# Performance work log

Measured on AMD Instinct MI355X. Metric: run time of the kernel, lower is better.

The kernel has to match this reference:

```python
import jax, jax.numpy as jnp
import numpy as np

INPUT_SIZE = 1024
HIDDEN_SIZE = 1024


def setup_inputs() -> dict:
    key = jax.random.key(0)
    k1, k2, k3 = jax.random.split(key, 3)
    x = jax.random.normal(k1, (512, 64, INPUT_SIZE), dtype=jnp.float32)
    weight_ih = jax.random.normal(k2, (INPUT_SIZE, HIDDEN_SIZE), dtype=jnp.float32)
    weight_hh = jax.random.normal(k3, (HIDDEN_SIZE, HIDDEN_SIZE), dtype=jnp.float32)
    return {"x": x, "weight_ih": weight_ih, "weight_hh": weight_hh}


def reference(x, weight_ih, weight_hh):
    # x: [T, B, input_size]; returns final hidden state [B, hidden_size]
    B = x.shape[1]
    h0 = jnp.zeros((B, weight_hh.shape[0]), dtype=x.dtype)

    def step(h, x_t):
        h = jnp.tanh(x_t @ weight_ih + h @ weight_hh)
        return h, None

    h_final, _ = jax.lax.scan(step, h0, x)
    return h_final
```

## Files before the change

### kernel.cpp

```cpp
#include <hip/hip_runtime.h>


#define TSTEPS 512
#define BATCH  64
#define HID    1024
#define NELEM  65536
#define LROW   1028

__device__ __forceinline__ float tanh_T2(float x) {
#pragma clang fp contract(off)
    const float C = 7.99881172180175781f;
    float ax = fabsf(x);
    float xc = fminf(fmaxf(x, -C), C);
    float x2 = xc * xc;
    float num = -2.76076847742355e-16f;
    num = __builtin_fmaf(x2, num, 2.00018790482477e-13f);
    num = __builtin_fmaf(x2, num, -8.60467152213735e-11f);
    num = __builtin_fmaf(x2, num, 5.12229709037114e-08f);
    num = __builtin_fmaf(x2, num, 1.48572235717979e-05f);
    num = __builtin_fmaf(x2, num, 6.37261928875436e-04f);
    num = __builtin_fmaf(x2, num, 4.89352455891786e-03f);
    num = xc * num;
    float den = 1.19825839466702e-06f;
    den = __builtin_fmaf(x2, den, 1.18534705686654e-04f);
    den = __builtin_fmaf(x2, den, 2.26843463243900e-03f);
    den = __builtin_fmaf(x2, den, 4.89352518554385e-03f);
    float r = num / den;
    return (ax < 0.0004f) ? x : r;
}

__global__ __launch_bounds__(256) void transpose_w(const float* __restrict__ W,
                                                   float* __restrict__ WT) {
    __shared__ float tile[64][65];
    const int c0 = blockIdx.x * 64;
    const int r0 = blockIdx.y * 64;
    const int tx = threadIdx.x & 63;
    const int ty = threadIdx.x >> 6;
    #pragma unroll
    for (int r = 0; r < 16; ++r) {
        const int rr = r * 4 + ty;
        tile[rr][tx] = W[(size_t)(r0 + rr) * HID + c0 + tx];
    }
    __syncthreads();
    #pragma unroll
    for (int r = 0; r < 16; ++r) {
        const int rr = r * 4 + ty;
        WT[(size_t)(c0 + rr) * HID + r0 + tx] = tile[tx][rr];
    }
}

__global__ __launch_bounds__(256, 2) void rnn_persist5(
    const float* __restrict__ x,
    const float* __restrict__ WTih,
    const float* __restrict__ WThh,
    float* __restrict__ hb0,
    float* __restrict__ hb1,
    unsigned int* __restrict__ cnt,
    float* __restrict__ out)
{
#pragma clang fp contract(off)
    __shared__ float lds_x[8 * LROW];
    __shared__ float lds_h[8 * LROW];
    __shared__ float pl[4][8][16];

    const int slice  = blockIdx.x & 7;
    const int wid    = blockIdx.x >> 3;
    const int bchunk = wid >> 3;
    const int jchunk = wid & 7;
    const int tid  = threadIdx.x;
    const int jl   = tid & 15;
    const int bp   = (tid >> 4) & 3;
    const int half = (tid >> 6) & 1;
    const int mat  = tid >> 7;
    const int jglob = slice * 128 + jchunk * 16 + jl;
    const int b0 = 2 * bp;

    const float* wrow = ((mat == 0) ? WTih : WThh)
                      + (size_t)jglob * HID + half * 512;
    float* hb[2] = { hb0, hb1 };
    unsigned int* mycnt = &cnt[bchunk * 32];

    for (int t = 0; t < TSTEPS; ++t) {
        float4 xv[8];
        {
            const float* xsrc = x + (size_t)t * NELEM
                              + (size_t)(bchunk * 8) * HID;
            #pragma unroll
            for (int u = 0; u < 8; ++u) {
                const int i = tid + u * 256;
                const int r = i >> 8, c4 = i & 255;
                xv[u] = ((const float4*)(xsrc + (size_t)r * HID))[c4];
            }
        }

        if (t > 0) {
            if (tid == 0) {
                const unsigned target = 64u * (unsigned)t;
                while (__hip_atomic_load(mycnt, __ATOMIC_RELAXED,
                                         __HIP_MEMORY_SCOPE_AGENT) < target)
                    __builtin_amdgcn_s_sleep(1);
            }
            __syncthreads();
        }

        #pragma unroll
        for (int u = 0; u < 8; ++u) {
            const int i = tid + u * 256;
            const int r = i >> 8, c4 = i & 255;
            *(float4*)&lds_x[r * LROW + c4 * 4] = xv[u];
        }
        if (t > 0) {
            const float* hsrc = hb[t & 1] + (size_t)(bchunk * 8) * HID;
            for (int blk = 0; blk < 4; ++blk) {
                float hv[8];
                #pragma unroll
                for (int u = 0; u < 8; ++u) {
                    const int i = tid + (blk * 8 + u) * 256;
                    const int r = i >> 10, k = i & 1023;
                    hv[u] = __hip_atomic_load(&hsrc[(size_t)r * HID + k],
                                              __ATOMIC_RELAXED,
                                              __HIP_MEMORY_SCOPE_AGENT);
                }
                #pragma unroll
                for (int u = 0; u < 8; ++u) {
                    const int i = tid + (blk * 8 + u) * 256;
                    const int r = i >> 10, k = i & 1023;
                    lds_h[r * LROW + k] = hv[u];
                }
            }
        }
        __syncthreads();

        float acc0 = 0.0f, acc1 = 0.0f;
        if (mat == 0 || t > 0) {
            const float* base = (mat == 0) ? lds_x : lds_h;
            const float* oa = base + b0 * LROW;
            const float* ob = base + (b0 + 1) * LROW;
            const float4* w4 = (const float4*)wrow;
            const int kbase = half * 512;
            #pragma unroll 4
            for (int kq = 0; kq < 128; ++kq) {
                const float4 w = w4[kq];
                const int k = kbase + kq * 4;
                acc0 = __builtin_fmaf(oa[k + 0], w.x, acc0);
                acc1 = __builtin_fmaf(ob[k + 0], w.x, acc1);
                acc0 = __builtin_fmaf(oa[k + 1], w.y, acc0);
                acc1 = __builtin_fmaf(ob[k + 1], w.y, acc1);
                acc0 = __builtin_fmaf(oa[k + 2], w.z, acc0);
                acc1 = __builtin_fmaf(ob[k + 2], w.z, acc1);
                acc0 = __builtin_fmaf(oa[k + 3], w.w, acc0);
                acc1 = __builtin_fmaf(ob[k + 3], w.w, acc1);
            }
        }
        pl[mat * 2 + half][b0][jl]     = acc0;
        pl[mat * 2 + half][b0 + 1][jl] = acc1;
        __syncthreads();

        if (tid < 128) {
            const int b = tid >> 4, j = tid & 15;
            const float dotX = pl[0][b][j] + pl[1][b][j];
            const float dotH = pl[2][b][j] + pl[3][b][j];
            const float hv = tanh_T2(dotX + dotH);
            const size_t o = (size_t)(bchunk * 8 + b) * HID
                           + (size_t)slice * 128 + (size_t)jchunk * 16 + j;
            if (t + 1 < TSTEPS)
                __hip_atomic_store(&hb[(t + 1) & 1][o], hv, __ATOMIC_RELAXED,
                                   __HIP_MEMORY_SCOPE_AGENT);
            else
                out[o] = hv;
        }
        __syncthreads();

        if (t + 1 < TSTEPS && tid == 0)
            __hip_atomic_fetch_add(mycnt, 1u, __ATOMIC_RELAXED,
                                   __HIP_MEMORY_SCOPE_AGENT);
    }
}

__global__ __launch_bounds__(256) void rnn_step_r8(
    const float* __restrict__ xt, const float* __restrict__ Wih,
    const float* __restrict__ Whh, const float* __restrict__ hin,
    float* __restrict__ hout)
{
#pragma clang fp contract(off)
    __shared__ float xs[4 * HID];
    __shared__ float hs[4 * HID];
    const int jb = blockIdx.x * 64;
    const int ib = blockIdx.y * 4;
    for (int idx = threadIdx.x; idx < 4 * HID; idx += 256) {
        xs[idx] = xt[ib * HID + idx];
        hs[idx] = hin ? hin[ib * HID + idx] : 0.0f;
    }
    __syncthreads();
    const int jl = threadIdx.x & 63;
    const int i  = threadIdx.x >> 6;
    const int j  = jb + jl;
    const float* xr = xs + i * HID;
    const float* hr = hs + i * HID;
    float cx0 = 0.f, cx1 = 0.f, ch0 = 0.f, ch1 = 0.f;
    #pragma unroll 8
    for (int k = 0; k < 512; ++k) {
        cx0 = __builtin_fmaf(xr[k], Wih[(size_t)k * HID + j], cx0);
        ch0 = __builtin_fmaf(hr[k], Whh[(size_t)k * HID + j], ch0);
    }
    #pragma unroll 8
    for (int k = 512; k < 1024; ++k) {
        cx1 = __builtin_fmaf(xr[k], Wih[(size_t)k * HID + j], cx1);
        ch1 = __builtin_fmaf(hr[k], Whh[(size_t)k * HID + j], ch1);
    }
    const float s = (cx0 + cx1) + (ch0 + ch1);
    hout[(size_t)(ib + i) * HID + j] = tanh_T2(s);
}

extern "C" void kernel_launch(void* const* d_in, const int* in_sizes, int n_in,
                              void* d_out, int out_size, void* d_ws, size_t ws_size,
                              hipStream_t stream) {
    const float* x   = (const float*)d_in[0];
    const float* Wih = (const float*)d_in[1];
    const float* Whh = (const float*)d_in[2];
    float* out = (float*)d_out;

    const size_t wT = (size_t)HID * HID;
    const size_t need = (2 * wT + 2 * (size_t)NELEM) * sizeof(float)
                      + 8 * 32 * sizeof(unsigned int);
    if (ws_size >= need) {
        float* WTih = (float*)d_ws;
        float* WThh = WTih + wT;
        float* hb0  = WThh + wT;
        float* hb1  = hb0 + NELEM;
        unsigned int* cnt = (unsigned int*)(hb1 + NELEM);

        transpose_w<<<dim3(16, 16), 256, 0, stream>>>(Wih, WTih);
        transpose_w<<<dim3(16, 16), 256, 0, stream>>>(Whh, WThh);
        hipMemsetAsync(cnt, 0, 8 * 32 * sizeof(unsigned int), stream);

        rnn_persist5<<<dim3(512), dim3(256), 0, stream>>>(
            x, WTih, WThh, hb0, hb1, cnt, out);
    } else {
        float* buf0 = (float*)d_ws;
        float* buf1 = buf0 + NELEM;
        const dim3 grid(HID / 64, BATCH / 4), block(256);
        for (int t = 0; t < TSTEPS; ++t) {
            const float* hin = (t == 0) ? nullptr
                              : ((t & 1) ? buf0 : buf1);
            float* hout = (t == TSTEPS - 1) ? out
                         : ((t & 1) ? buf1 : buf0);
            rnn_step_r8<<<grid, block, 0, stream>>>(
                x + (size_t)t * NELEM, Wih, Whh, hin, hout);
        }
    }
}
```

Before: 16.27 ms.

## Hoist input projection into a batched GEMM before the persistent recurrent kernel

Computes x_t @ W_ih for all timesteps up front in a separate parallel GEMM kernel, writing a large dotX buffer to workspace. The persistent recurrent kernel then only does the h @ W_hh matvec per step, reading precomputed dotX, with a new 256-block by 512-thread layout. This takes the input projection off the serial critical path, at the cost of 128MB of extra workspace traffic. The old per-step fallback is removed, and the previous persistent kernel now serves as the fallback when workspace is too small.

```diff
diff --git a/kernel.cpp b/kernel.cpp
--- a/kernel.cpp
+++ b/kernel.cpp
@@ -49,13 +49,166 @@
     }
 }
 
-__global__ __launch_bounds__(256, 2) void rnn_persist5(
+__global__ __launch_bounds__(256) void gemm_x(
     const float* __restrict__ x,
-    const float* __restrict__ WTih,
+    const float* __restrict__ Wih,
+    float* __restrict__ dotX)
+{
+#pragma clang fp contract(off)
+    __shared__ float xs[16 * LROW];
+
+    const int t  = blockIdx.z;
+    const int bc = blockIdx.y;
+    const int jb = blockIdx.x * 64;
+    const int tid = threadIdx.x;
+
+    {
+        const float* xsrc = x + (size_t)t * NELEM + (size_t)(bc * 16) * HID;
+        #pragma unroll
+        for (int s = 0; s < 16; ++s) {
+            const int f = tid + s * 256;
+            const int r = f >> 8, c4 = f & 255;
+            const float4 v = ((const float4*)(xsrc + (size_t)r * HID))[c4];
+            *(float4*)&xs[r * LROW + c4 * 4] = v;
+        }
+    }
+    __syncthreads();
+
+    const int jq = tid & 15;
+    const int i  = tid >> 4;
+    const int j0 = jb + jq * 4;
+    const float* xr = xs + i * LROW;
+
+    float a0[4] = {0.f, 0.f, 0.f, 0.f};
+    float a1[4] = {0.f, 0.f, 0.f, 0.f};
+    #pragma unroll 8
+    for (int k = 0; k < 512; ++k) {
+        const float4 w = *(const float4*)(Wih + (size_t)k * HID + j0);
+        const float xv = xr[k];
+        a0[0] = __builtin_fmaf(xv, w.x, a0[0]);
+        a0[1] = __builtin_fmaf(xv, w.y, a0[1]);
+        a0[2] = __builtin_fmaf(xv, w.z, a0[2]);
+        a0[3] = __builtin_fmaf(xv, w.w, a0[3]);
+    }
+    #pragma unroll 8
+    for (int k = 512; k < 1024; ++k) {
+        const float4 w = *(const float4*)(Wih + (size_t)k * HID + j0);
+        const float xv = xr[k];
+        a1[0] = __builtin_fmaf(xv, w.x, a1[0]);
+        a1[1] = __builtin_fmaf(xv, w.y, a1[1]);
+        a1[2] = __builtin_fmaf(xv, w.z, a1[2]);
+        a1[3] = __builtin_fmaf(xv, w.w, a1[3]);
+    }
+    float4 r;
+    r.x = a0[0] + a1[0];
+    r.y = a0[1] + a1[1];
+    r.z = a0[2] + a1[2];
+    r.w = a0[3] + a1[3];
+    *(float4*)(dotX + (size_t)t * NELEM + (size_t)(bc * 16 + i) * HID + j0) = r;
+}
+
+__global__ __launch_bounds__(512, 1) void rnn_persist7(
+    const float* __restrict__ dotX,
     const float* __restrict__ WThh,
     float* __restrict__ hb0,
     float* __restrict__ hb1,
     unsigned int* __restrict__ cnt,
+    float* __restrict__ out)
+{
+#pragma clang fp contract(off)
+    __shared__ float lds_h[8 * LROW];
+    __shared__ float pl[2][8][32];
+
+    const int xcd    = blockIdx.x & 7;
+    const int jsub   = (blockIdx.x >> 3) & 3;
+    const int bchunk = blockIdx.x >> 5;
+    const int tid  = threadIdx.x;
+    const int jl   = tid & 31;
+    const int b    = (tid >> 5) & 7;
+    const int half = tid >> 8;
+    const int jbase = xcd * 128 + jsub * 32;
+    const int j     = jbase + jl;
+
+    const float* wrow = WThh + (size_t)j * HID + half * 512;
+    float* hb[2] = { hb0, hb1 };
+    unsigned int* mycnt = &cnt[bchunk * 32];
+
+    for (int t = 0; t < TSTEPS; ++t) {
+        float dxv = 0.0f;
+        if (tid < 256) {
+            const int cb = tid >> 5, cj = tid & 31;
+            dxv = dotX[(size_t)t * NELEM + (size_t)(bchunk * 8 + cb) * HID
+                       + jbase + cj];
+        }
+
+        if (t > 0) {
+            if (tid == 0) {
+                const unsigned target = 32u * (unsigned)t;
+                while (__hip_atomic_load(mycnt, __ATOMIC_RELAXED,
+                                         __HIP_MEMORY_SCOPE_AGENT) < target)
+                    __builtin_amdgcn_s_sleep(1);
+            }
+            __syncthreads();
+
+            const float* hsrc = hb[t & 1] + (size_t)(bchunk * 8) * HID;
+            float hv[16];
+            #pragma unroll
+            for (int u = 0; u < 16; ++u) {
+                const int i = tid + u * 512;
+                const int r = i >> 10, k = i & 1023;
+                hv[u] = __hip_atomic_load(&hsrc[(size_t)r * HID + k],
+                                          __ATOMIC_RELAXED,
+                                          __HIP_MEMORY_SCOPE_AGENT);
+            }
+            #pragma unroll
+            for (int u = 0; u < 16; ++u) {
+                const int i = tid + u * 512;
+                const int r = i >> 10, k = i & 1023;
+                lds_h[r * LROW + k] = hv[u];
+            }
+        }
+        __syncthreads();
+
+        float acc = 0.0f;
+        if (t > 0) {
+            const float* hrow = lds_h + b * LROW + half * 512;
+            const float4* w4 = (const float4*)wrow;
+            #pragma unroll 4
+            for (int kq = 0; kq < 128; ++kq) {
+                const float4 w = w4[kq];
+                const int k = kq * 4;
+                acc = __builtin_fmaf(hrow[k + 0], w.x, acc);
+                acc = __builtin_fmaf(hrow[k + 1], w.y, acc);
+                acc = __builtin_fmaf(hrow[k + 2], w.z, acc);
+                acc = __builtin_fmaf(hrow[k + 3], w.w, acc);
+            }
+        }
+        pl[half][b][jl] = acc;
+        __syncthreads();
+
+        if (tid < 256) {
+            const int cb = tid >> 5, cj = tid & 31;
+            const float dotH = pl[0][cb][cj] + pl[1][cb][cj];
+            const float hv = tanh_T2(dxv + dotH);
+            const size_t o = (size_t)(bchunk * 8 + cb) * HID + jbase + cj;
+            if (t + 1 < TSTEPS)
+                __hip_atomic_store(&hb[(t + 1) & 1][o], hv, __ATOMIC_RELAXED,
+                                   __HIP_MEMORY_SCOPE_AGENT);
+            else
+                out[o] = hv;
+        }
+        __syncthreads();
+
+        if (t + 1 < TSTEPS && tid == 0)
+            __hip_atomic_fetch_add(mycnt, 1u, __ATOMIC_RELAXED,
+                                   __HIP_MEMORY_SCOPE_AGENT);
+    }
+}
+
+__global__ __launch_bounds__(256, 2) void rnn_persist5(
+    const float* __restrict__ x, const float* __restrict__ WTih,
+    const float* __restrict__ WThh, float* __restrict__ hb0,
+    float* __restrict__ hb1, unsigned int* __restrict__ cnt,
     float* __restrict__ out)
 {
 #pragma clang fp contract(off)
@@ -92,7 +245,6 @@
                 xv[u] = ((const float4*)(xsrc + (size_t)r * HID))[c4];
             }
         }
-
         if (t > 0) {
             if (tid == 0) {
                 const unsigned target = 64u * (unsigned)t;
@@ -102,7 +254,6 @@
             }
             __syncthreads();
         }
-
         #pragma unroll
         for (int u = 0; u < 8; ++u) {
             const int i = tid + u * 256;
@@ -177,41 +328,6 @@
     }
 }
 
-__global__ __launch_bounds__(256) void rnn_step_r8(
-    const float* __restrict__ xt, const float* __restrict__ Wih,
-    const float* __restrict__ Whh, const float* __restrict__ hin,
-    float* __restrict__ hout)
-{
-#pragma clang fp contract(off)
-    __shared__ float xs[4 * HID];
-    __shared__ float hs[4 * HID];
-    const int jb = blockIdx.x * 64;
-    const int ib = blockIdx.y * 4;
-    for (int idx = threadIdx.x; idx < 4 * HID; idx += 256) {
-        xs[idx] = xt[ib * HID + idx];
-        hs[idx] = hin ? hin[ib * HID + idx] : 0.0f;
-    }
-    __syncthreads();
-    const int jl = threadIdx.x & 63;
-    const int i  = threadIdx.x >> 6;
-    const int j  = jb + jl;
-    const float* xr = xs + i * HID;
-    const float* hr = hs + i * HID;
-    float cx0 = 0.f, cx1 = 0.f, ch0 = 0.f, ch1 = 0.f;
-    #pragma unroll 8
-    for (int k = 0; k < 512; ++k) {
-        cx0 = __builtin_fmaf(xr[k], Wih[(size_t)k * HID + j], cx0);
-        ch0 = __builtin_fmaf(hr[k], Whh[(size_t)k * HID + j], ch0);
-    }
-    #pragma unroll 8
-    for (int k = 512; k < 1024; ++k) {
-        cx1 = __builtin_fmaf(xr[k], Wih[(size_t)k * HID + j], cx1);
-        ch1 = __builtin_fmaf(hr[k], Whh[(size_t)k * HID + j], ch1);
-    }
-    const float s = (cx0 + cx1) + (ch0 + ch1);
-    hout[(size_t)(ib + i) * HID + j] = tanh_T2(s);
-}
-
 extern "C" void kernel_launch(void* const* d_in, const int* in_sizes, int n_in,
                               void* d_out, int out_size, void* d_ws, size_t ws_size,
                               hipStream_t stream) {
@@ -220,33 +336,36 @@
     const float* Whh = (const float*)d_in[2];
     float* out = (float*)d_out;
 
-    const size_t wT = (size_t)HID * HID;
-    const size_t need = (2 * wT + 2 * (size_t)NELEM) * sizeof(float)
-                      + 8 * 32 * sizeof(unsigned int);
-    if (ws_size >= need) {
+    const size_t dotX_f = (size_t)TSTEPS * NELEM;
+    const size_t wT_f   = (size_t)HID * HID;
+    const size_t need_new = (dotX_f + wT_f + 2 * (size_t)NELEM) * sizeof(float)
+                          + 8 * 32 * sizeof(unsigned int);
+    const size_t need_old = (2 * wT_f + 2 * (size_t)NELEM) * sizeof(float)
+                          + 8 * 32 * sizeof(unsigned int);
+
+    if (ws_size >= need_new) {
+        float* dotX = (float*)d_ws;
+        float* WThh = dotX + dotX_f;
+        float* hb0  = WThh + wT_f;
+        float* hb1  = hb0 + NELEM;
+        unsigned int* cnt = (unsigned int*)(hb1 + NELEM);
+
+        transpose_w<<<dim3(16, 16), 256, 0, stream>>>(Whh, WThh);
+        gemm_x<<<dim3(16, 4, TSTEPS), 256, 0, stream>>>(x, Wih, dotX);
+        hipMemsetAsync(cnt, 0, 8 * 32 * sizeof(unsigned int), stream);
+        rnn_persist7<<<dim3(256), dim3(512), 0, stream>>>(
+            dotX, WThh, hb0, hb1, cnt, out);
+    } else {
         float* WTih = (float*)d_ws;
-        float* WThh = WTih + wT;
-        float* hb0  = WThh + wT;
+        float* WThh = WTih + wT_f;
+        float* hb0  = WThh + wT_f;
         float* hb1  = hb0 + NELEM;
         unsigned int* cnt = (unsigned int*)(hb1 + NELEM);
 
         transpose_w<<<dim3(16, 16), 256, 0, stream>>>(Wih, WTih);
         transpose_w<<<dim3(16, 16), 256, 0, stream>>>(Whh, WThh);
         hipMemsetAsync(cnt, 0, 8 * 32 * sizeof(unsigned int), stream);
-
         rnn_persist5<<<dim3(512), dim3(256), 0, stream>>>(
             x, WTih, WThh, hb0, hb1, cnt, out);
-    } else {
-        float* buf0 = (float*)d_ws;
-        float* buf1 = buf0 + NELEM;
-        const dim3 grid(HID / 64, BATCH / 4), block(256);
-        for (int t = 0; t < TSTEPS; ++t) {
-            const float* hin = (t == 0) ? nullptr
-                              : ((t & 1) ? buf0 : buf1);
-            float* hout = (t == TSTEPS - 1) ? out
-                         : ((t & 1) ? buf1 : buf0);
-            rnn_step_r8<<<grid, block, 0, stream>>>(
-                x + (size_t)t * NELEM, Wih, Whh, hin, hout);
-        }
-    }
-}
+    }
+}
```

New measurement: 19.16 ms. 1.18x slower.
